# Kernel optimization log

Measured on AMD Instinct MI355X. Metric: run time of the kernel, lower is better.

Reference implementation:

```python
import jax, jax.numpy as jnp
import numpy as np

EPS = 1e-08   # CanberraDistLayer eps (max(1e-8, 1e-8))
N_POW = 1.0   # similarity exponent
MAX_DIST = 1000000.0


def setup_inputs() -> dict:
    key = jax.random.key(0)
    k1, k2, k3, k4 = jax.random.split(key, 4)
    B, D_IN, H, OUT = 1024, 1024, 512, 512
    x = jax.random.normal(k1, (B, D_IN), dtype=jnp.float32)
    W1 = jax.random.normal(k2, (H, D_IN), dtype=jnp.float32) * 0.02  # MLP weight (torch Linear layout [out,in])
    b1 = jax.random.normal(k3, (H,), dtype=jnp.float32) * 0.02
    Wd = jax.random.normal(k4, (OUT, H), dtype=jnp.float32)          # dist-layer prototype rows
    return {"x": x, "W1": W1, "b1": b1, "Wd": Wd}


def reference(x, W1, b1, Wd):
    # MLP trunk: Linear + ReLU  -> hidden features h: [B, H]
    h = jax.nn.relu(jnp.einsum("bd,hd->bh", x, W1) + b1)
    # Canberra distance (variant='standard') of each hidden vector vs each weight row.
    # Broadcast to [B, OUT, H]; reduce over feature dim H.
    he = h[:, None, :]          # [B, 1, H]
    we = Wd[None, :, :]         # [1, OUT, H]
    numerator = jnp.abs(he - we)
    denominator = jnp.abs(he) + jnp.abs(we)
    denominator = jnp.where(denominator < EPS, EPS, denominator)
    canberra_dist = jnp.sum(numerator / denominator, axis=-1)  # [B, OUT]
    # scale=False path
    dist_clamped = jnp.clip(canberra_dist + EPS, EPS, MAX_DIST)
    similarity = dist_clamped ** (-N_POW)
    return similarity
```

## Files before the change

kernel.cpp:

```cpp
#include <hip/hip_runtime.h>
#include <hip/hip_fp16.h>

#define DIN 1024
#define H_SZ 512
#define OUT_SZ 512
#define EPSF 1e-8f

typedef __attribute__((ext_vector_type(8))) short short8v;
typedef __attribute__((ext_vector_type(4))) float f32x4;
typedef _Float16 half2v __attribute__((ext_vector_type(2)));

static __device__ inline unsigned short f2bf(float f) {
    unsigned u = __float_as_uint(f);
    u = u + 0x7FFFu + ((u >> 16) & 1u);
    return (unsigned short)(u >> 16);
}

static __device__ inline void canb2(unsigned hu, unsigned wu, unsigned& a, unsigned two) {
    unsigned mn, sm, tt, y;
    asm("v_pk_min_f16 %0, %1, %2" : "=v"(mn) : "v"(hu), "v"(wu));
    asm("v_pk_add_f16 %0, %1, %2" : "=v"(sm) : "v"(hu), "v"(wu));
    y = 0x77847784u - sm;
    asm("v_pk_fma_f16 %0, %1, %2, %3 neg_lo:[1,0,0] neg_hi:[1,0,0]"
        : "=v"(tt) : "v"(sm), "v"(y), "v"(two));
    asm("v_pk_mul_f16 %0, %1, %2" : "=v"(y) : "v"(y), "v"(tt));
    asm("v_pk_fma_f16 %0, %1, %2, %0" : "+v"(a) : "v"(mn), "v"(y));
}

__global__ __launch_bounds__(512, 4) void gemm8(const float* __restrict__ x,
                                                const float* __restrict__ W1,
                                                const float* __restrict__ b1,
                                                const float* __restrict__ Wd,
                                                unsigned short* __restrict__ hh,
                                                unsigned short* __restrict__ wh) {
    __shared__ unsigned short As[2][2][32][72];
    __shared__ unsigned short Bs[2][2][32][72];
    __shared__ float red[4][64][4];
    const int t  = threadIdx.x;
    const int b0 = blockIdx.x * 32;
    const int o0 = blockIdx.y * 32;

    const int w  = t >> 6;
    const int l  = t & 63;
    const int q  = w & 3;
    const int kh = w >> 2;
    const int m0 = (q >> 1) * 16;
    const int n0 = (q & 1) * 16;
    const int lr = l & 15;
    const int lk = (l >> 4) * 8;
    const int th = t & 255;
    const int ar = th >> 3;
    const int ko = (th & 7) * 8;

    f32x4 acc = {0.f, 0.f, 0.f, 0.f};
    const float* arow = &x [(size_t)(b0 + ar) * DIN + kh * 512 + ko];
    const float* brow = &W1[(size_t)(o0 + ar) * DIN + kh * 512 + ko];
    float4 pa0 = *reinterpret_cast<const float4*>(arow);
    float4 pa1 = *reinterpret_cast<const float4*>(arow + 4);
    float4 pb0 = *reinterpret_cast<const float4*>(brow);
    float4 pb1 = *reinterpret_cast<const float4*>(brow + 4);

    for (int k0 = 0; k0 < 512; k0 += 64) {
        const int buf = (k0 >> 6) & 1;
        short8v av, bv;
        av[0] = (short)f2bf(pa0.x); av[1] = (short)f2bf(pa0.y);
        av[2] = (short)f2bf(pa0.z); av[3] = (short)f2bf(pa0.w);
        av[4] = (short)f2bf(pa1.x); av[5] = (short)f2bf(pa1.y);
        av[6] = (short)f2bf(pa1.z); av[7] = (short)f2bf(pa1.w);
        bv[0] = (short)f2bf(pb0.x); bv[1] = (short)f2bf(pb0.y);
        bv[2] = (short)f2bf(pb0.z); bv[3] = (short)f2bf(pb0.w);
        bv[4] = (short)f2bf(pb1.x); bv[5] = (short)f2bf(pb1.y);
        bv[6] = (short)f2bf(pb1.z); bv[7] = (short)f2bf(pb1.w);
        *reinterpret_cast<short8v*>(&As[kh][buf][ar][ko]) = av;
        *reinterpret_cast<short8v*>(&Bs[kh][buf][ar][ko]) = bv;
        __syncthreads();
        if (k0 + 64 < 512) {
            pa0 = *reinterpret_cast<const float4*>(arow + k0 + 64);
            pa1 = *reinterpret_cast<const float4*>(arow + k0 + 68);
            pb0 = *reinterpret_cast<const float4*>(brow + k0 + 64);
            pb1 = *reinterpret_cast<const float4*>(brow + k0 + 68);
        }
        #pragma unroll
        for (int s = 0; s < 2; ++s) {
            const short8v af = *reinterpret_cast<const short8v*>(&As[kh][buf][m0 + lr][s * 32 + lk]);
            const short8v bf = *reinterpret_cast<const short8v*>(&Bs[kh][buf][n0 + lr][s * 32 + lk]);
            acc = __builtin_amdgcn_mfma_f32_16x16x32_bf16(af, bf, acc, 0, 0, 0);
        }
    }
    __syncthreads();
    if (kh == 1) {
        #pragma unroll
        for (int r = 0; r < 4; ++r) red[q][l][r] = acc[r];
    }
    __syncthreads();
    if (kh == 0) {
        const int col = o0 + n0 + lr;
        const float bias = b1[col];
        #pragma unroll
        for (int r = 0; r < 4; ++r) {
            const float v = acc[r] + red[q][l][r] + bias;
            const int m = b0 + m0 + (l >> 4) * 4 + r;
            hh[(size_t)m * H_SZ + col] = __half_as_ushort(__float2half(fmaxf(v, 0.0f)));
        }
    }
    const int gid = (blockIdx.y * 32 + blockIdx.x) * 512 + t;
    const float wv0 = Wd[gid];
    wh[gid] = __half_as_ushort(__float2half(wv0 > 0.f ? wv0 : 0.f));
}

#define LDg(g_, hv_, wv_) do {                                                   \
    const int col_ = base + (g_) * 4;                                            \
    _Pragma("unroll") for (int c_ = 0; c_ < 4; ++c_)                             \
        hv_[c_] = *reinterpret_cast<const uint4*>(&hs[bi + 8 * c_][col_]);       \
    _Pragma("unroll") for (int d_ = 0; d_ < 2; ++d_)                             \
        wv_[d_] = *reinterpret_cast<const uint4*>(&ws_[oj + 16 * d_][col_]);     \
} while (0)

#define CMPg(hv_, wv_) do {                                                      \
    _Pragma("unroll") for (int c_ = 0; c_ < 4; ++c_)                             \
        _Pragma("unroll") for (int d_ = 0; d_ < 2; ++d_) {                       \
            canb2(hv_[c_].x, wv_[d_].x, acc[c_][d_], two);                       \
            canb2(hv_[c_].y, wv_[d_].y, acc[c_][d_], two);                       \
            canb2(hv_[c_].z, wv_[d_].z, acc[c_][d_], two);                       \
            canb2(hv_[c_].w, wv_[d_].w, acc[c_][d_], two);                       \
        }                                                                        \
} while (0)

__global__ __launch_bounds__(512, 4) void canberra5(const unsigned short* __restrict__ hh,
                                                    const unsigned short* __restrict__ wh,
                                                    float* __restrict__ out) {
    __shared__ unsigned hs[32][260];
    __shared__ unsigned ws_[32][260];
    const int t = threadIdx.x;
    const int b0 = blockIdx.x * 32;
    const int o0 = blockIdx.y * 32;
    const unsigned* hu = reinterpret_cast<const unsigned*>(hh);
    const unsigned* wu = reinterpret_cast<const unsigned*>(wh);

    #pragma unroll
    for (int r = 0; r < 4; ++r) {
        const int s = t + r * 512;
        const int row = s >> 6;
        const int c16 = s & 63;
        *reinterpret_cast<uint4*>(&hs[row][c16 * 4]) =
            *reinterpret_cast<const uint4*>(&hu[(size_t)(b0 + row) * 256 + c16 * 4]);
        *reinterpret_cast<uint4*>(&ws_[row][c16 * 4]) =
            *reinterpret_cast<const uint4*>(&wu[(size_t)(o0 + row) * 256 + c16 * 4]);
    }
    __syncthreads();

    const int ks = t >> 7;
    const int ts = t & 127;
    const int bi = ts >> 4;
    const int oj = ts & 15;
    const unsigned two = 0x40004000u;

    unsigned acc[4][2] = {};
    const int base = ks * 64;

    uint4 hA[4], wA[2], hB[4], wB[2];
    LDg(0, hA, wA);
    #pragma unroll 2
    for (int g = 0; g < 16; g += 2) {
        LDg(g + 1, hB, wB);
        CMPg(hA, wA);
        if (g + 2 < 16) LDg(g + 2, hA, wA);
        CMPg(hB, wB);
    }

    float p[8];
    #pragma unroll
    for (int c = 0; c < 4; ++c)
        #pragma unroll
        for (int d = 0; d < 2; ++d) {
            const half2v av = __builtin_bit_cast(half2v, acc[c][d]);
            p[c * 2 + d] = (float)av.x + (float)av.y;
        }

    __syncthreads();
    float* red = reinterpret_cast<float*>(&hs[0][0]);
    if (ks > 0) {
        const int slot = (ks - 1) * 128 + ts;
        #pragma unroll
        for (int i = 0; i < 8; ++i) red[i * 384 + slot] = p[i];
    }
    __syncthreads();
    if (ks == 0) {
        #pragma unroll
        for (int q = 0; q < 3; ++q) {
            #pragma unroll
            for (int i = 0; i < 8; ++i) p[i] += red[i * 384 + q * 128 + ts];
        }
        #pragma unroll
        for (int c = 0; c < 4; ++c) {
            #pragma unroll
            for (int d = 0; d < 2; ++d) {
                float dd = 512.0f - 2.0f * p[c * 2 + d] + EPSF;
                dd = fminf(fmaxf(dd, EPSF), 1000000.0f);
                out[(size_t)(b0 + bi + 8 * c) * OUT_SZ + o0 + oj + 16 * d] = 1.0f / dd;
            }
        }
    }
}

extern "C" void kernel_launch(void* const* d_in, const int* in_sizes, int n_in,
                              void* d_out, int out_size, void* d_ws, size_t ws_size,
                              hipStream_t stream) {
    const float* x  = (const float*)d_in[0];
    const float* W1 = (const float*)d_in[1];
    const float* b1 = (const float*)d_in[2];
    const float* Wd = (const float*)d_in[3];
    float* out = (float*)d_out;
    unsigned short* hh = (unsigned short*)d_ws;
    unsigned short* wh = (unsigned short*)((char*)d_ws + (1u << 20));

    gemm8<<<dim3(32, 16), 512, 0, stream>>>(x, W1, b1, Wd, hh, wh);
    canberra5<<<dim3(32, 16), 512, 0, stream>>>(hh, wh, out);
}
```

Before: 39.94 us.

## Shrink canberra tile to 32x16 and stream the feature dimension in two chunks

Rewrites the Canberra kernel to use 32x16 output tiles with a doubled grid, and loads the hidden/weight rows into shared memory in two 128-word chunks instead of all at once. The split-K factor goes from 4 to 8 slices per block. Shared memory per block drops and the launch-bounds hint rises to 8 blocks per CU, aimed at better occupancy and more blocks to cover the GPU. In exchange it adds an extra barrier per chunk, a larger cross-slice reduction, lower data reuse per tile, and drops the software double-buffering of LDS reads.

Result: no change. 40.04 us (+0.3%).

```diff
diff --git a/kernel.cpp b/kernel.cpp
--- a/kernel.cpp
+++ b/kernel.cpp
@@ -108,64 +108,64 @@
     wh[gid] = __half_as_ushort(__float2half(wv0 > 0.f ? wv0 : 0.f));
 }
 
-#define LDg(g_, hv_, wv_) do {                                                   \
-    const int col_ = base + (g_) * 4;                                            \
-    _Pragma("unroll") for (int c_ = 0; c_ < 4; ++c_)                             \
-        hv_[c_] = *reinterpret_cast<const uint4*>(&hs[bi + 8 * c_][col_]);       \
-    _Pragma("unroll") for (int d_ = 0; d_ < 2; ++d_)                             \
-        wv_[d_] = *reinterpret_cast<const uint4*>(&ws_[oj + 16 * d_][col_]);     \
-} while (0)
-
-#define CMPg(hv_, wv_) do {                                                      \
-    _Pragma("unroll") for (int c_ = 0; c_ < 4; ++c_)                             \
-        _Pragma("unroll") for (int d_ = 0; d_ < 2; ++d_) {                       \
-            canb2(hv_[c_].x, wv_[d_].x, acc[c_][d_], two);                       \
-            canb2(hv_[c_].y, wv_[d_].y, acc[c_][d_], two);                       \
-            canb2(hv_[c_].z, wv_[d_].z, acc[c_][d_], two);                       \
-            canb2(hv_[c_].w, wv_[d_].w, acc[c_][d_], two);                       \
-        }                                                                        \
-} while (0)
-
-__global__ __launch_bounds__(512, 4) void canberra5(const unsigned short* __restrict__ hh,
+__global__ __launch_bounds__(512, 8) void canberra6(const unsigned short* __restrict__ hh,
                                                     const unsigned short* __restrict__ wh,
                                                     float* __restrict__ out) {
-    __shared__ unsigned hs[32][260];
-    __shared__ unsigned ws_[32][260];
-    const int t = threadIdx.x;
+    __shared__ unsigned hs[32][132];
+    __shared__ unsigned ws[16][132];
+    const int t  = threadIdx.x;
     const int b0 = blockIdx.x * 32;
-    const int o0 = blockIdx.y * 32;
+    const int o0 = blockIdx.y * 16;
     const unsigned* hu = reinterpret_cast<const unsigned*>(hh);
     const unsigned* wu = reinterpret_cast<const unsigned*>(wh);
 
-    #pragma unroll
-    for (int r = 0; r < 4; ++r) {
-        const int s = t + r * 512;
-        const int row = s >> 6;
-        const int c16 = s & 63;
-        *reinterpret_cast<uint4*>(&hs[row][c16 * 4]) =
-            *reinterpret_cast<const uint4*>(&hu[(size_t)(b0 + row) * 256 + c16 * 4]);
-        *reinterpret_cast<uint4*>(&ws_[row][c16 * 4]) =
-            *reinterpret_cast<const uint4*>(&wu[(size_t)(o0 + row) * 256 + c16 * 4]);
-    }
-    __syncthreads();
-
-    const int ks = t >> 7;
-    const int ts = t & 127;
-    const int bi = ts >> 4;
-    const int oj = ts & 15;
+    const int ks = t >> 6;
+    const int l  = t & 63;
+    const int bi = l >> 3;
+    const int oj = l & 7;
     const unsigned two = 0x40004000u;
 
     unsigned acc[4][2] = {};
-    const int base = ks * 64;
-
-    uint4 hA[4], wA[2], hB[4], wB[2];
-    LDg(0, hA, wA);
-    #pragma unroll 2
-    for (int g = 0; g < 16; g += 2) {
-        LDg(g + 1, hB, wB);
-        CMPg(hA, wA);
-        if (g + 2 < 16) LDg(g + 2, hA, wA);
-        CMPg(hB, wB);
+
+    for (int ch = 0; ch < 2; ++ch) {
+        if (ch) __syncthreads();
+        #pragma unroll
+        for (int r = 0; r < 2; ++r) {
+            const int s = t + r * 512;
+            const int row = s >> 5;
+            const int c4  = s & 31;
+            *reinterpret_cast<uint4*>(&hs[row][c4 * 4]) =
+                *reinterpret_cast<const uint4*>(&hu[(size_t)(b0 + row) * 256 + ch * 128 + c4 * 4]);
+        }
+        {
+            const int row = t >> 5;
+            const int c4  = t & 31;
+            *reinterpret_cast<uint4*>(&ws[row][c4 * 4]) =
+                *reinterpret_cast<const uint4*>(&wu[(size_t)(o0 + row) * 256 + ch * 128 + c4 * 4]);
+        }
+        __syncthreads();
+
+        #pragma unroll
+        for (int g = 0; g < 4; ++g) {
+            const int col = ks * 16 + g * 4;
+            uint4 hv[4], wv[2];
+            #pragma unroll
+            for (int c = 0; c < 4; ++c)
+                hv[c] = *reinterpret_cast<const uint4*>(&hs[bi + 8 * c][col]);
+            #pragma unroll
+            for (int d = 0; d < 2; ++d)
+                wv[d] = *reinterpret_cast<const uint4*>(&ws[oj + 8 * d][col]);
+            #pragma unroll
+            for (int c = 0; c < 4; ++c) {
+                #pragma unroll
+                for (int d = 0; d < 2; ++d) {
+                    canb2(hv[c].x, wv[d].x, acc[c][d], two);
+                    canb2(hv[c].y, wv[d].y, acc[c][d], two);
+                    canb2(hv[c].z, wv[d].z, acc[c][d], two);
+                    canb2(hv[c].w, wv[d].w, acc[c][d], two);
+                }
+            }
+        }
     }
 
     float p[8];
@@ -180,16 +180,16 @@
     __syncthreads();
     float* red = reinterpret_cast<float*>(&hs[0][0]);
     if (ks > 0) {
-        const int slot = (ks - 1) * 128 + ts;
-        #pragma unroll
-        for (int i = 0; i < 8; ++i) red[i * 384 + slot] = p[i];
+        const int slot = (ks - 1) * 64 + l;
+        #pragma unroll
+        for (int i = 0; i < 8; ++i) red[i * 448 + slot] = p[i];
     }
     __syncthreads();
     if (ks == 0) {
         #pragma unroll
-        for (int q = 0; q < 3; ++q) {
-            #pragma unroll
-            for (int i = 0; i < 8; ++i) p[i] += red[i * 384 + q * 128 + ts];
+        for (int q = 0; q < 7; ++q) {
+            #pragma unroll
+            for (int i = 0; i < 8; ++i) p[i] += red[i * 448 + q * 64 + l];
         }
         #pragma unroll
         for (int c = 0; c < 4; ++c) {
@@ -197,7 +197,7 @@
             for (int d = 0; d < 2; ++d) {
                 float dd = 512.0f - 2.0f * p[c * 2 + d] + EPSF;
                 dd = fminf(fmaxf(dd, EPSF), 1000000.0f);
-                out[(size_t)(b0 + bi + 8 * c) * OUT_SZ + o0 + oj + 16 * d] = 1.0f / dd;
+                out[(size_t)(b0 + bi + 8 * c) * OUT_SZ + o0 + oj + 8 * d] = 1.0f / dd;
             }
         }
     }
@@ -215,5 +215,5 @@
     unsigned short* wh = (unsigned short*)((char*)d_ws + (1u << 20));
 
     gemm8<<<dim3(32, 16), 512, 0, stream>>>(x, W1, b1, Wd, hh, wh);
-    canberra5<<<dim3(32, 16), 512, 0, stream>>>(hh, wh, out);
-}
+    canberra6<<<dim3(32, 32), 512, 0, stream>>>(hh, wh, out);
+}
```
